# Optimization experiments

Measured on AMD Instinct MI355X. Metric: run time of the kernel, lower is better.

Reference implementation:

```python
import jax, jax.numpy as jnp
import numpy as np

N_HEAD, D_MODEL, D_K, D_V = 16, 1024, 64, 64
B, L = 8, 1024
LN_EPS = 1e-5
NEG_INF = -1e9


def setup_inputs() -> dict:
    key = jax.random.key(0)
    ks = jax.random.split(key, 12)
    s = 0.02
    return {
        "q": jax.random.normal(ks[0], (B, L, D_MODEL), jnp.float32),
        "k": jax.random.normal(ks[1], (B, L, D_MODEL), jnp.float32),
        "v": jax.random.normal(ks[2], (B, L, D_MODEL), jnp.float32),
        "mask": jnp.zeros((B, L, L), dtype=bool),
        "wq": jax.random.normal(ks[3], (D_MODEL, N_HEAD * D_K), jnp.float32) * s,
        "bq": jnp.zeros((N_HEAD * D_K,), jnp.float32),
        "wk": jax.random.normal(ks[4], (D_MODEL, N_HEAD * D_K), jnp.float32) * s,
        "bk": jnp.zeros((N_HEAD * D_K,), jnp.float32),
        "wv": jax.random.normal(ks[5], (D_MODEL, N_HEAD * D_V), jnp.float32) * s,
        "bv": jnp.zeros((N_HEAD * D_V,), jnp.float32),
        "wo": jax.random.normal(ks[6], (N_HEAD * D_V, D_MODEL), jnp.float32) * s,
        "bo": jnp.zeros((D_MODEL,), jnp.float32),
        "gamma": jnp.ones((D_MODEL,), jnp.float32),
        "beta": jnp.zeros((D_MODEL,), jnp.float32),
    }


def reference(q, k, v, mask, wq, bq, wk, bk, wv, bv, wo, bo, gamma, beta):
    b, lq, _ = q.shape
    lk = k.shape[1]
    residual = q
    # separate Q/K/V projections, split heads: [b, len, h, d]
    qh = (q @ wq + bq).reshape(b, lq, N_HEAD, D_K)
    kh = (k @ wk + bk).reshape(b, lk, N_HEAD, D_K)
    vh = (v @ wv + bv).reshape(b, lk, N_HEAD, D_V)
    # scaled dot-product attention (temperature = sqrt(d_k))
    scores = jnp.einsum("bqhd,bkhd->bhqk", qh, kh) / jnp.sqrt(jnp.float32(D_K))
    scores = jnp.where(mask[:, None, :, :], NEG_INF, scores)
    attn = jax.nn.softmax(scores, axis=-1)  # [b, h, lq, lk]
    ctx = jnp.einsum("bhqk,bkhd->bqhd", attn, vh).reshape(b, lq, N_HEAD * D_V)
    # out-proj (dropout is identity in eval) + residual + LayerNorm
    out = ctx @ wo + bo + residual
    mu = out.mean(-1, keepdims=True)
    var = out.var(-1, keepdims=True)
    out = (out - mu) * jax.lax.rsqrt(var + LN_EPS) * gamma + beta
    # match original attn layout: [n_head*b, lq, lk]
    attn_flat = attn.transpose(1, 0, 2, 3).reshape(N_HEAD * b, lq, lk)
    return out, attn_flat
```

## Files before the change

kernel.cpp:

```cpp
#include <hip/hip_runtime.h>
#include <stdint.h>

static constexpr int BATCH  = 8;
static constexpr int SEQ    = 1024;
static constexpr int DMODEL = 1024;
static constexpr int NHEAD  = 16;

typedef __attribute__((ext_vector_type(8))) short sh8;
typedef __attribute__((ext_vector_type(4))) float fl4;

__device__ __forceinline__ uint16_t f2bf(float f) {
    union { float f; uint32_t u; } a; a.f = f;
    uint32_t r = a.u + 0x7FFFu + ((a.u >> 16) & 1u);
    return (uint16_t)(r >> 16);
}

__device__ __forceinline__ float b2f(uint16_t u) {
    union { uint32_t u; float f; } a; a.u = ((uint32_t)u) << 16; return a.f;
}

__device__ __forceinline__ sh8 pack_bf8(fl4 x0, fl4 x1) {
    union { uint16_t u[8]; sh8 v; } pk;
    pk.u[0] = f2bf(x0[0]); pk.u[1] = f2bf(x0[1]); pk.u[2] = f2bf(x0[2]); pk.u[3] = f2bf(x0[3]);
    pk.u[4] = f2bf(x1[0]); pk.u[5] = f2bf(x1[1]); pk.u[6] = f2bf(x1[2]); pk.u[7] = f2bf(x1[3]);
    return pk.v;
}

__device__ __forceinline__ fl4 mfma16(sh8 a, sh8 b, fl4 c) {
    return __builtin_amdgcn_mfma_f32_16x16x32_bf16(a, b, c, 0, 0, 0);
}

__device__ __forceinline__ void gload16(const void* g, void* l) {
    __builtin_amdgcn_global_load_lds(
        (const __attribute__((address_space(1))) void*)g,
        (__attribute__((address_space(3))) void*)l, 16, 0, 0);
}

__global__ __launch_bounds__(256) void cvt3_kernel(const float* __restrict__ q,
                                                   const float* __restrict__ k,
                                                   const float* __restrict__ v,
                                                   uint16_t* __restrict__ dq,
                                                   uint16_t* __restrict__ dk,
                                                   uint16_t* __restrict__ dv) {
    const int z = blockIdx.z;
    const float* src = (z == 0) ? q : (z == 1) ? k : v;
    uint16_t* dst = (z == 0) ? dq : (z == 1) ? dk : dv;
    const int t = blockIdx.x * 256 + threadIdx.x;
    #pragma unroll
    for (int it = 0; it < 2; ++it) {
        const int i = (it * 524288 + t) * 8;
        fl4 x0 = *(const fl4*)(src + i), x1 = *(const fl4*)(src + i + 4);
        *(sh8*)(dst + i) = pack_bf8(x0, x1);
    }
}

__global__ __launch_bounds__(256) void wtrans_kernel(const float* __restrict__ wq, const float* __restrict__ wk,
                                                     const float* __restrict__ wv, const float* __restrict__ wo,
                                                     uint16_t* __restrict__ tq, uint16_t* __restrict__ tk,
                                                     uint16_t* __restrict__ tv, uint16_t* __restrict__ to) {
    __shared__ uint16_t T[64][72];
    const int z = blockIdx.z;
    const float* w = (z == 0) ? wq : (z == 1) ? wk : (z == 2) ? wv : wo;
    uint16_t* wT = (z == 0) ? tq : (z == 1) ? tk : (z == 2) ? tv : to;
    const int n0 = blockIdx.x * 64, k0 = blockIdx.y * 64;
    const int tid = threadIdx.x;
    #pragma unroll
    for (int it = 0; it < 4; ++it) {
        int g = it * 256 + tid;
        int r = g >> 4, c = (g & 15) * 4;
        fl4 x = *(const fl4*)(w + (size_t)(k0 + r) * DMODEL + n0 + c);
        T[r][c + 0] = f2bf(x[0]); T[r][c + 1] = f2bf(x[1]);
        T[r][c + 2] = f2bf(x[2]); T[r][c + 3] = f2bf(x[3]);
    }
    __syncthreads();
    #pragma unroll
    for (int it = 0; it < 4; ++it) {
        int g = it * 256 + tid;
        int r = g >> 4, c = (g & 15) * 4;
        ushort4 o;
        o.x = T[c + 0][r]; o.y = T[c + 1][r]; o.z = T[c + 2][r]; o.w = T[c + 3][r];
        *(ushort4*)(wT + (size_t)(n0 + r) * DMODEL + k0 + c) = o;
    }
}

__global__ __launch_bounds__(256) void vtrans_kernel(const uint16_t* __restrict__ vh,
                                                     uint16_t* __restrict__ vT) {
    __shared__ uint16_t T[64][72];
    const int l0 = blockIdx.x * 64, hd0 = blockIdx.y * 64, bb = blockIdx.z;
    const uint16_t* src = vh + (size_t)bb * SEQ * DMODEL;
    uint16_t* dst = vT + (size_t)bb * SEQ * DMODEL;
    const int tid = threadIdx.x;
    #pragma unroll
    for (int it = 0; it < 4; ++it) {
        int g = it * 256 + tid;
        int r = g >> 4, c = (g & 15) * 4;
        ushort4 x = *(const ushort4*)(src + (size_t)(l0 + r) * DMODEL + hd0 + c);
        T[r][c + 0] = x.x; T[r][c + 1] = x.y; T[r][c + 2] = x.z; T[r][c + 3] = x.w;
    }
    __syncthreads();
    #pragma unroll
    for (int it = 0; it < 4; ++it) {
        int g = it * 256 + tid;
        int r = g >> 4, c = (g & 15) * 4;
        ushort4 o;
        o.x = T[c + 0][r]; o.y = T[c + 1][r]; o.z = T[c + 2][r]; o.w = T[c + 3][r];
        *(ushort4*)(dst + (size_t)(hd0 + r) * DMODEL + l0 + c) = o;
    }
}

template<bool OUT_BF16, bool RESID>
__device__ __forceinline__
void gemm_body(const uint16_t* __restrict__ Ab, const uint16_t* __restrict__ Bt,
               const float* __restrict__ bias, const float* __restrict__ resid,
               void* __restrict__ Cv, int m0, int n0,
               uint16_t* Alds, uint16_t* Blds) {
    const int tid = threadIdx.x;
    const int lane = tid & 63, wid = tid >> 6;
    const int wr = (wid >> 1) * 64, wc = (wid & 1) * 64;
    const int fr = lane & 15, fk = (lane >> 4) * 8;

    fl4 acc[4][4];
    #pragma unroll
    for (int i = 0; i < 4; ++i)
        #pragma unroll
        for (int j = 0; j < 4; ++j) acc[i][j] = (fl4){0.f, 0.f, 0.f, 0.f};

    for (int kt = 0; kt < 16; ++kt) {
        const int kb = kt * 64;
        #pragma unroll
        for (int it = 0; it < 4; ++it) {
            const int g = it * 256 + tid;
            const int r = g >> 3, c = (g & 7) << 3;
            const int lofs = __builtin_amdgcn_readfirstlane((it * 256 + wid * 64) * 16);
            gload16(Ab + (size_t)(m0 + r) * DMODEL + kb + c, (char*)Alds + lofs);
            gload16(Bt + (size_t)(n0 + r) * DMODEL + kb + c, (char*)Blds + lofs);
        }
        __syncthreads();
        #pragma unroll
        for (int ks = 0; ks < 2; ++ks) {
            sh8 a[4], bb[4];
            #pragma unroll
            for (int mi = 0; mi < 4; ++mi) a[mi] = *(const sh8*)&Alds[(wr + mi * 16 + fr) * 64 + ks * 32 + fk];
            #pragma unroll
            for (int ni = 0; ni < 4; ++ni) bb[ni] = *(const sh8*)&Blds[(wc + ni * 16 + fr) * 64 + ks * 32 + fk];
            #pragma unroll
            for (int mi = 0; mi < 4; ++mi)
                #pragma unroll
                for (int ni = 0; ni < 4; ++ni) acc[mi][ni] = mfma16(a[mi], bb[ni], acc[mi][ni]);
        }
        __syncthreads();
    }

    #pragma unroll
    for (int mi = 0; mi < 4; ++mi) {
        #pragma unroll
        for (int ni = 0; ni < 4; ++ni) {
            const int col = n0 + wc + ni * 16 + fr;
            const float bv = bias[col];
            #pragma unroll
            for (int i = 0; i < 4; ++i) {
                const int row = m0 + wr + mi * 16 + (lane >> 4) * 4 + i;
                float val = acc[mi][ni][i] + bv;
                if (RESID) val += resid[(size_t)row * DMODEL + col];
                if (OUT_BF16) ((uint16_t*)Cv)[(size_t)row * DMODEL + col] = f2bf(val);
                else          ((float*)Cv)[(size_t)row * DMODEL + col] = val;
            }
        }
    }
}

__global__ __launch_bounds__(256)
void gemm_proj(const uint16_t* __restrict__ A0, const uint16_t* __restrict__ A1, const uint16_t* __restrict__ A2,
               const uint16_t* __restrict__ B0, const uint16_t* __restrict__ B1, const uint16_t* __restrict__ B2,
               const float* __restrict__ b0, const float* __restrict__ b1, const float* __restrict__ b2,
               uint16_t* __restrict__ C0, uint16_t* __restrict__ C1, uint16_t* __restrict__ C2) {
    __shared__ uint16_t Alds[128 * 64];
    __shared__ uint16_t Blds[128 * 64];
    const int z = blockIdx.z;
    const uint16_t* Ab = (z == 0) ? A0 : (z == 1) ? A1 : A2;
    const uint16_t* Bt = (z == 0) ? B0 : (z == 1) ? B1 : B2;
    const float* bias  = (z == 0) ? b0 : (z == 1) ? b1 : b2;
    uint16_t* Cv       = (z == 0) ? C0 : (z == 1) ? C1 : C2;
    gemm_body<true, false>(Ab, Bt, bias, nullptr, Cv, blockIdx.y * 128, blockIdx.x * 128, Alds, Blds);
}

__global__ __launch_bounds__(256)
void gemm_out(const uint16_t* __restrict__ Ab, const uint16_t* __restrict__ Bt,
              const float* __restrict__ bias, const float* __restrict__ resid,
              float* __restrict__ Cv) {
    __shared__ uint16_t Alds[128 * 64];
    __shared__ uint16_t Blds[128 * 64];
    gemm_body<false, true>(Ab, Bt, bias, resid, Cv, blockIdx.y * 128, blockIdx.x * 128, Alds, Blds);
}

__global__ __launch_bounds__(256)
void attn_kernel(const uint16_t* __restrict__ qh, const uint16_t* __restrict__ kh,
                 const uint16_t* __restrict__ vT, const uint8_t* __restrict__ mask,
                 float* __restrict__ attn, uint16_t* __restrict__ ctx) {
    __shared__ uint16_t S[16 * 1024];
    __shared__ float rinv[16];
    const int q0 = blockIdx.x * 16, h = blockIdx.y, b = blockIdx.z;
    const int tid = threadIdx.x, lane = tid & 63, wid = tid >> 6;
    const int fr = lane & 15, fk = (lane >> 4) * 8, frow4 = (lane >> 4) * 4;

    sh8 Aq[2];
    #pragma unroll
    for (int ks = 0; ks < 2; ++ks)
        Aq[ks] = *(const sh8*)(qh + (size_t)(b * SEQ + q0 + fr) * DMODEL + h * 64 + ks * 32 + fk);

    for (int t8 = 0; t8 < 8; ++t8) {
        const int kv0 = (t8 * 4 + wid) * 32;
        sh8 Bk[2][2];
        #pragma unroll
        for (int ni = 0; ni < 2; ++ni)
            #pragma unroll
            for (int ks = 0; ks < 2; ++ks)
                Bk[ni][ks] = *(const sh8*)(kh + (size_t)(b * SEQ + kv0 + ni * 16 + fr) * DMODEL + h * 64 + ks * 32 + fk);
        fl4 sa[2];
        #pragma unroll
        for (int ni = 0; ni < 2; ++ni) sa[ni] = (fl4){0.f, 0.f, 0.f, 0.f};
        #pragma unroll
        for (int ni = 0; ni < 2; ++ni)
            #pragma unroll
            for (int ks = 0; ks < 2; ++ks) sa[ni] = mfma16(Aq[ks], Bk[ni][ks], sa[ni]);
        #pragma unroll
        for (int ni = 0; ni < 2; ++ni)
            #pragma unroll
            for (int i = 0; i < 4; ++i) {
                const int row = frow4 + i, col = kv0 + ni * 16 + fr;
                S[row * 1024 + ((((col >> 3) ^ (row & 15)) << 3) | (col & 7))] = f2bf(sa[ni][i] * 0.125f);
            }
    }
    __syncthreads();

    {
        const int r = tid >> 4, j = tid & 15;
        const int rbase = r * 1024;
        const uint8_t* mbase = mask + (size_t)(b * SEQ + q0 + r) * SEQ;
        sh8 sv[8];
        float mx = -1e30f;
        #pragma unroll
        for (int c4 = 0; c4 < 8; ++c4) {
            const int cc = c4 * 16 + j;
            sh8 x = *(sh8*)&S[rbase + ((cc ^ r) << 3)];
            const uint2 mw = *(const uint2*)(mbase + cc * 8);
            union { uint16_t u[8]; sh8 v; } o;
            #pragma unroll
            for (int t = 0; t < 4; ++t) {
                float f = b2f((uint16_t)x[t]);
                if ((mw.x >> (t * 8)) & 0xFF) f = -1e9f;
                o.u[t] = f2bf(f);
                mx = fmaxf(mx, f);
            }
            #pragma unroll
            for (int t = 0; t < 4; ++t) {
                float f = b2f((uint16_t)x[4 + t]);
                if ((mw.y >> (t * 8)) & 0xFF) f = -1e9f;
                o.u[4 + t] = f2bf(f);
                mx = fmaxf(mx, f);
            }
            sv[c4] = o.v;
        }
        #pragma unroll
        for (int d = 1; d < 16; d <<= 1) mx = fmaxf(mx, __shfl_xor(mx, d));
        float sum = 0.f;
        #pragma unroll
        for (int c4 = 0; c4 < 8; ++c4) {
            const int cc = c4 * 16 + j;
            union { uint16_t u[8]; sh8 v; } o;
            #pragma unroll
            for (int t = 0; t < 8; ++t) {
                float e = __expf(b2f((uint16_t)sv[c4][t]) - mx);
                o.u[t] = f2bf(e);
                sum += e;
            }
            sv[c4] = o.v;
            *(sh8*)&S[rbase + ((cc ^ r) << 3)] = o.v;
        }
        #pragma unroll
        for (int d = 1; d < 16; d <<= 1) sum += __shfl_xor(sum, d);
        const float ri = 1.f / sum;
        if (j == 0) rinv[r] = ri;
        float* ab = attn + ((size_t)((h * BATCH + b) * SEQ + q0 + r)) * SEQ;
        #pragma unroll
        for (int c4 = 0; c4 < 8; ++c4) {
            const int cc = c4 * 16 + j;
            fl4 o0, o1;
            #pragma unroll
            for (int t = 0; t < 4; ++t) o0[t] = b2f((uint16_t)sv[c4][t]) * ri;
            #pragma unroll
            for (int t = 0; t < 4; ++t) o1[t] = b2f((uint16_t)sv[c4][4 + t]) * ri;
            float* dst = ab + cc * 8;
            __builtin_nontemporal_store(o0, (fl4*)dst);
            __builtin_nontemporal_store(o1, (fl4*)(dst + 4));
        }
    }
    __syncthreads();

    fl4 acc0 = (fl4){0.f, 0.f, 0.f, 0.f}, acc1 = (fl4){0.f, 0.f, 0.f, 0.f};
    const uint16_t* vbase = vT + (size_t)((b * NHEAD + h) * 64 + wid * 16) * SEQ;
    const int frx = fr & 15;
    #pragma unroll 4
    for (int ks2 = 0; ks2 < 32; ++ks2) {
        const int kv = ks2 * 32;
        sh8 Ap = *(const sh8*)&S[fr * 1024 + ((((kv + fk) >> 3) ^ frx) << 3)];
        sh8 Bv = *(const sh8*)(vbase + (size_t)fr * SEQ + kv + fk);
        if (ks2 & 1) acc1 = mfma16(Ap, Bv, acc1);
        else         acc0 = mfma16(Ap, Bv, acc0);
    }
    #pragma unroll
    for (int i = 0; i < 4; ++i) {
        const int q = frow4 + i;
        const float val = (acc0[i] + acc1[i]) * rinv[q];
        ctx[(size_t)(b * SEQ + q0 + q) * DMODEL + h * 64 + wid * 16 + fr] = f2bf(val);
    }
}

__global__ __launch_bounds__(256)
void ln_kernel(const float* __restrict__ raw, const float* __restrict__ gamma,
               const float* __restrict__ beta, float* __restrict__ out) {
    const int row = blockIdx.x;
    const int tid = threadIdx.x;
    const float* x = raw + (size_t)row * DMODEL;
    fl4 xv = *(const fl4*)(x + tid * 4);
    float s  = xv[0] + xv[1] + xv[2] + xv[3];
    float ss = xv[0] * xv[0] + xv[1] * xv[1] + xv[2] * xv[2] + xv[3] * xv[3];
    #pragma unroll
    for (int d = 1; d < 64; d <<= 1) { s += __shfl_xor(s, d); ss += __shfl_xor(ss, d); }
    __shared__ float sb[4], ssb[4];
    if ((tid & 63) == 0) { sb[tid >> 6] = s; ssb[tid >> 6] = ss; }
    __syncthreads();
    s  = sb[0] + sb[1] + sb[2] + sb[3];
    ss = ssb[0] + ssb[1] + ssb[2] + ssb[3];
    const float mu  = s * (1.f / 1024.f);
    const float var = ss * (1.f / 1024.f) - mu * mu;
    const float rstd = rsqrtf(var + 1e-5f);
    fl4 g  = *(const fl4*)(gamma + tid * 4);
    fl4 be = *(const fl4*)(beta + tid * 4);
    fl4 o;
    #pragma unroll
    for (int j = 0; j < 4; ++j) o[j] = (xv[j] - mu) * rstd * g[j] + be[j];
    *(fl4*)(out + (size_t)row * DMODEL + tid * 4) = o;
}

extern "C" void kernel_launch(void* const* d_in, const int* in_sizes, int n_in,
                              void* d_out, int out_size, void* d_ws, size_t ws_size,
                              hipStream_t stream) {
    (void)in_sizes; (void)n_in; (void)out_size; (void)ws_size;
    const float* q     = (const float*)d_in[0];
    const float* k     = (const float*)d_in[1];
    const float* v     = (const float*)d_in[2];
    const uint8_t* mask = (const uint8_t*)d_in[3];
    const float* wq = (const float*)d_in[4];
    const float* bq = (const float*)d_in[5];
    const float* wk = (const float*)d_in[6];
    const float* bk = (const float*)d_in[7];
    const float* wv = (const float*)d_in[8];
    const float* bv = (const float*)d_in[9];
    const float* wo = (const float*)d_in[10];
    const float* bo = (const float*)d_in[11];
    const float* gamma = (const float*)d_in[12];
    const float* beta  = (const float*)d_in[13];

    float* out  = (float*)d_out;
    float* attn = out + (size_t)BATCH * SEQ * DMODEL;

    uint16_t* qcvt = (uint16_t*)(attn);
    uint16_t* kcvt = (uint16_t*)((char*)attn + ((size_t)16 << 20));
    uint16_t* vcvt = (uint16_t*)((char*)attn + ((size_t)32 << 20));

    char* ws = (char*)d_ws;
    uint16_t* qh   = (uint16_t*)(ws);
    uint16_t* kh   = (uint16_t*)(ws + ((size_t)16 << 20));
    uint16_t* vT   = (uint16_t*)(ws + ((size_t)32 << 20));
    uint16_t* ctx  = (uint16_t*)(ws + ((size_t)48 << 20));
    uint16_t* wqT  = (uint16_t*)(ws + ((size_t)64 << 20));
    uint16_t* wkT  = (uint16_t*)(ws + ((size_t)66 << 20));
    uint16_t* wvT  = (uint16_t*)(ws + ((size_t)68 << 20));
    uint16_t* woT  = (uint16_t*)(ws + ((size_t)70 << 20));
    uint16_t* vtmp = (uint16_t*)(ws + ((size_t)72 << 20));

    dim3 tb(256);
    wtrans_kernel<<<dim3(16, 16, 4), tb, 0, stream>>>(wq, wk, wv, wo, wqT, wkT, wvT, woT);
    cvt3_kernel<<<dim3(2048, 1, 3), tb, 0, stream>>>(q, k, v, qcvt, kcvt, vcvt);

    gemm_proj<<<dim3(8, 64, 3), tb, 0, stream>>>(qcvt, kcvt, vcvt, wqT, wkT, wvT,
                                                 bq, bk, bv, qh, kh, vtmp);

    vtrans_kernel<<<dim3(16, 16, 8), tb, 0, stream>>>(vtmp, vT);

    attn_kernel<<<dim3(64, NHEAD, BATCH), tb, 0, stream>>>(qh, kh, vT, mask, attn, ctx);

    gemm_out<<<dim3(8, 64), tb, 0, stream>>>(ctx, woT, bo, q, out);

    ln_kernel<<<BATCH * SEQ, tb, 0, stream>>>(out, gamma, beta, out);
}
```

Baseline: 456.4 us.

## Fold softmax scale into Wq, use packed bf16 convert, reorder grid mappings

Folds the 1/sqrt(d_k) scale into the Wq weights and bias at conversion time, so the attention kernel no longer multiplies every score. Replaces the manual bf16 rounding in pack_bf8 and the softmax exp path with the v_cvt_pk_bf16_f32 instruction. Restructures the softmax so masked scores are recomputed from the raw values instead of being rounded to bf16 and stored in between. Swaps the grid dimension order for the projection, attention and output GEMM launches, which changes block scheduling order and L2 locality. Scaling the weights before bf16 rounding shifts the rounding point slightly.

New measurement: 455.2 us. No clear change (-0.3%).

```diff
diff --git a/kernel.cpp b/kernel.cpp
--- a/kernel.cpp
+++ b/kernel.cpp
@@ -19,10 +19,16 @@
     union { uint32_t u; float f; } a; a.u = ((uint32_t)u) << 16; return a.f;
 }
 
+__device__ __forceinline__ uint32_t cvtpk(float lo, float hi) {
+    uint32_t r;
+    asm("v_cvt_pk_bf16_f32 %0, %1, %2" : "=v"(r) : "v"(lo), "v"(hi));
+    return r;
+}
+
 __device__ __forceinline__ sh8 pack_bf8(fl4 x0, fl4 x1) {
-    union { uint16_t u[8]; sh8 v; } pk;
-    pk.u[0] = f2bf(x0[0]); pk.u[1] = f2bf(x0[1]); pk.u[2] = f2bf(x0[2]); pk.u[3] = f2bf(x0[3]);
-    pk.u[4] = f2bf(x1[0]); pk.u[5] = f2bf(x1[1]); pk.u[6] = f2bf(x1[2]); pk.u[7] = f2bf(x1[3]);
+    union { uint32_t w[4]; sh8 v; } pk;
+    pk.w[0] = cvtpk(x0[0], x0[1]); pk.w[1] = cvtpk(x0[2], x0[3]);
+    pk.w[2] = cvtpk(x1[0], x1[1]); pk.w[3] = cvtpk(x1[2], x1[3]);
     return pk.v;
 }
 
@@ -62,6 +68,7 @@
     const int z = blockIdx.z;
     const float* w = (z == 0) ? wq : (z == 1) ? wk : (z == 2) ? wv : wo;
     uint16_t* wT = (z == 0) ? tq : (z == 1) ? tk : (z == 2) ? tv : to;
+    const float ws = (z == 0) ? 0.125f : 1.f;
     const int n0 = blockIdx.x * 64, k0 = blockIdx.y * 64;
     const int tid = threadIdx.x;
     #pragma unroll
@@ -69,8 +76,8 @@
         int g = it * 256 + tid;
         int r = g >> 4, c = (g & 15) * 4;
         fl4 x = *(const fl4*)(w + (size_t)(k0 + r) * DMODEL + n0 + c);
-        T[r][c + 0] = f2bf(x[0]); T[r][c + 1] = f2bf(x[1]);
-        T[r][c + 2] = f2bf(x[2]); T[r][c + 3] = f2bf(x[3]);
+        T[r][c + 0] = f2bf(x[0] * ws); T[r][c + 1] = f2bf(x[1] * ws);
+        T[r][c + 2] = f2bf(x[2] * ws); T[r][c + 3] = f2bf(x[3] * ws);
     }
     __syncthreads();
     #pragma unroll
@@ -111,7 +118,7 @@
 template<bool OUT_BF16, bool RESID>
 __device__ __forceinline__
 void gemm_body(const uint16_t* __restrict__ Ab, const uint16_t* __restrict__ Bt,
-               const float* __restrict__ bias, const float* __restrict__ resid,
+               const float* __restrict__ bias, float bscale, const float* __restrict__ resid,
                void* __restrict__ Cv, int m0, int n0,
                uint16_t* Alds, uint16_t* Blds) {
     const int tid = threadIdx.x;
@@ -156,7 +163,7 @@
         #pragma unroll
         for (int ni = 0; ni < 4; ++ni) {
             const int col = n0 + wc + ni * 16 + fr;
-            const float bv = bias[col];
+            const float bv = bias[col] * bscale;
             #pragma unroll
             for (int i = 0; i < 4; ++i) {
                 const int row = m0 + wr + mi * 16 + (lane >> 4) * 4 + i;
@@ -181,7 +188,8 @@
     const uint16_t* Bt = (z == 0) ? B0 : (z == 1) ? B1 : B2;
     const float* bias  = (z == 0) ? b0 : (z == 1) ? b1 : b2;
     uint16_t* Cv       = (z == 0) ? C0 : (z == 1) ? C1 : C2;
-    gemm_body<true, false>(Ab, Bt, bias, nullptr, Cv, blockIdx.y * 128, blockIdx.x * 128, Alds, Blds);
+    const float bs     = (z == 0) ? 0.125f : 1.f;
+    gemm_body<true, false>(Ab, Bt, bias, bs, nullptr, Cv, blockIdx.x * 128, blockIdx.y * 128, Alds, Blds);
 }
 
 __global__ __launch_bounds__(256)
@@ -190,7 +198,7 @@
               float* __restrict__ Cv) {
     __shared__ uint16_t Alds[128 * 64];
     __shared__ uint16_t Blds[128 * 64];
-    gemm_body<false, true>(Ab, Bt, bias, resid, Cv, blockIdx.y * 128, blockIdx.x * 128, Alds, Blds);
+    gemm_body<false, true>(Ab, Bt, bias, 1.f, resid, Cv, blockIdx.x * 128, blockIdx.y * 128, Alds, Blds);
 }
 
 __global__ __launch_bounds__(256)
@@ -199,7 +207,7 @@
                  float* __restrict__ attn, uint16_t* __restrict__ ctx) {
     __shared__ uint16_t S[16 * 1024];
     __shared__ float rinv[16];
-    const int q0 = blockIdx.x * 16, h = blockIdx.y, b = blockIdx.z;
+    const int b = blockIdx.x, h = blockIdx.y, q0 = blockIdx.z * 16;
     const int tid = threadIdx.x, lane = tid & 63, wid = tid >> 6;
     const int fr = lane & 15, fk = (lane >> 4) * 8, frow4 = (lane >> 4) * 4;
 
@@ -228,7 +236,7 @@
             #pragma unroll
             for (int i = 0; i < 4; ++i) {
                 const int row = frow4 + i, col = kv0 + ni * 16 + fr;
-                S[row * 1024 + ((((col >> 3) ^ (row & 15)) << 3) | (col & 7))] = f2bf(sa[ni][i] * 0.125f);
+                S[row * 1024 + ((((col >> 3) ^ (row & 15)) << 3) | (col & 7))] = f2bf(sa[ni][i]);
             }
     }
     __syncthreads();
@@ -237,45 +245,49 @@
         const int r = tid >> 4, j = tid & 15;
         const int rbase = r * 1024;
         const uint8_t* mbase = mask + (size_t)(b * SEQ + q0 + r) * SEQ;
-        sh8 sv[8];
+        sh8 x[8];
+        uint2 mw[8];
         float mx = -1e30f;
         #pragma unroll
         for (int c4 = 0; c4 < 8; ++c4) {
             const int cc = c4 * 16 + j;
-            sh8 x = *(sh8*)&S[rbase + ((cc ^ r) << 3)];
-            const uint2 mw = *(const uint2*)(mbase + cc * 8);
-            union { uint16_t u[8]; sh8 v; } o;
+            x[c4] = *(sh8*)&S[rbase + ((cc ^ r) << 3)];
+            mw[c4] = *(const uint2*)(mbase + cc * 8);
             #pragma unroll
             for (int t = 0; t < 4; ++t) {
-                float f = b2f((uint16_t)x[t]);
-                if ((mw.x >> (t * 8)) & 0xFF) f = -1e9f;
-                o.u[t] = f2bf(f);
+                float f = ((mw[c4].x >> (t * 8)) & 0xFF) ? -1e9f : b2f((uint16_t)x[c4][t]);
                 mx = fmaxf(mx, f);
             }
             #pragma unroll
             for (int t = 0; t < 4; ++t) {
-                float f = b2f((uint16_t)x[4 + t]);
-                if ((mw.y >> (t * 8)) & 0xFF) f = -1e9f;
-                o.u[4 + t] = f2bf(f);
+                float f = ((mw[c4].y >> (t * 8)) & 0xFF) ? -1e9f : b2f((uint16_t)x[c4][4 + t]);
                 mx = fmaxf(mx, f);
             }
-            sv[c4] = o.v;
         }
         #pragma unroll
         for (int d = 1; d < 16; d <<= 1) mx = fmaxf(mx, __shfl_xor(mx, d));
         float sum = 0.f;
+        sh8 sv[8];
         #pragma unroll
         for (int c4 = 0; c4 < 8; ++c4) {
             const int cc = c4 * 16 + j;
-            union { uint16_t u[8]; sh8 v; } o;
-            #pragma unroll
-            for (int t = 0; t < 8; ++t) {
-                float e = __expf(b2f((uint16_t)sv[c4][t]) - mx);
-                o.u[t] = f2bf(e);
-                sum += e;
-            }
-            sv[c4] = o.v;
-            *(sh8*)&S[rbase + ((cc ^ r) << 3)] = o.v;
+            float e[8];
+            #pragma unroll
+            for (int t = 0; t < 4; ++t) {
+                float f = ((mw[c4].x >> (t * 8)) & 0xFF) ? -1e9f : b2f((uint16_t)x[c4][t]);
+                e[t] = __expf(f - mx);
+            }
+            #pragma unroll
+            for (int t = 0; t < 4; ++t) {
+                float f = ((mw[c4].y >> (t * 8)) & 0xFF) ? -1e9f : b2f((uint16_t)x[c4][4 + t]);
+                e[4 + t] = __expf(f - mx);
+            }
+            union { uint32_t w[4]; sh8 v; } pk;
+            pk.w[0] = cvtpk(e[0], e[1]); pk.w[1] = cvtpk(e[2], e[3]);
+            pk.w[2] = cvtpk(e[4], e[5]); pk.w[3] = cvtpk(e[6], e[7]);
+            sv[c4] = pk.v;
+            *(sh8*)&S[rbase + ((cc ^ r) << 3)] = pk.v;
+            sum += e[0] + e[1] + e[2] + e[3] + e[4] + e[5] + e[6] + e[7];
         }
         #pragma unroll
         for (int d = 1; d < 16; d <<= 1) sum += __shfl_xor(sum, d);
@@ -384,14 +396,14 @@
     wtrans_kernel<<<dim3(16, 16, 4), tb, 0, stream>>>(wq, wk, wv, wo, wqT, wkT, wvT, woT);
     cvt3_kernel<<<dim3(2048, 1, 3), tb, 0, stream>>>(q, k, v, qcvt, kcvt, vcvt);
 
-    gemm_proj<<<dim3(8, 64, 3), tb, 0, stream>>>(qcvt, kcvt, vcvt, wqT, wkT, wvT,
+    gemm_proj<<<dim3(64, 8, 3), tb, 0, stream>>>(qcvt, kcvt, vcvt, wqT, wkT, wvT,
                                                  bq, bk, bv, qh, kh, vtmp);
 
     vtrans_kernel<<<dim3(16, 16, 8), tb, 0, stream>>>(vtmp, vT);
 
-    attn_kernel<<<dim3(64, NHEAD, BATCH), tb, 0, stream>>>(qh, kh, vT, mask, attn, ctx);
-
-    gemm_out<<<dim3(8, 64), tb, 0, stream>>>(ctx, woT, bo, q, out);
+    attn_kernel<<<dim3(BATCH, NHEAD, 64), tb, 0, stream>>>(qh, kh, vT, mask, attn, ctx);
+
+    gemm_out<<<dim3(64, 8), tb, 0, stream>>>(ctx, woT, bo, q, out);
 
     ln_kernel<<<BATCH * SEQ, tb, 0, stream>>>(out, gamma, beta, out);
 }
```
